# Kernel optimization log

Hardware: AMD Instinct MI355X
Metric: run time of the kernel (lower is better)

The kernel has to match this reference:

```python
import jax, jax.numpy as jnp
import numpy as np

N1 = 4096
N2 = 4096


def _encoder(x, w1, b1, w2, b2, w3, b3):
    # fc1 -> fc2 -> fc3 -> relu (relu only after fc3, matching the torch code)
    h = x @ w1.T + b1
    h = h @ w2.T + b2
    h = h @ w3.T + b3
    return jax.nn.relu(h)


def _self_attention(x, adj, alpha, W):
    # tmp_i = sum_j [adj_ij==1] * alpha_ij * W * x_j ; tmp_i /= deg_i ; tmp_i += x_i (only if deg_i != 0)
    a = (adj == 1).astype(x.dtype)          # [N, N]
    deg = a.sum(axis=1)                     # [N]
    agg = (a * alpha) @ x                   # [N, 64] masked weighted aggregation
    agg = agg * W[0, 0]
    safe_deg = jnp.maximum(deg, 1.0)
    out = agg / safe_deg[:, None] + x       # residual
    return jnp.where((deg != 0.0)[:, None], out, jnp.zeros_like(out))


def setup_inputs() -> dict:
    key = jax.random.key(0)
    ks = jax.random.split(key, 20)
    s = 0.02  # weight scale to keep activations sane through the 4096->256->128->64 MLP
    inp = {
        "x1": jax.random.normal(ks[0], (N1, N1), jnp.float32),
        "x2": jax.random.normal(ks[1], (N2, N2), jnp.float32),
        "adj1": jax.random.randint(ks[2], (N1, N1), 0, 2, jnp.int32),
        "adj2": jax.random.randint(ks[3], (N2, N2), 0, 2, jnp.int32),
        "e1_w1": jax.random.normal(ks[4], (256, N1), jnp.float32) * s,
        "e1_b1": jnp.zeros((256,), jnp.float32),
        "e1_w2": jax.random.normal(ks[5], (128, 256), jnp.float32) * s,
        "e1_b2": jnp.zeros((128,), jnp.float32),
        "e1_w3": jax.random.normal(ks[6], (64, 128), jnp.float32) * s,
        "e1_b3": jnp.zeros((64,), jnp.float32),
        "e2_w1": jax.random.normal(ks[7], (256, N2), jnp.float32) * s,
        "e2_b1": jnp.zeros((256,), jnp.float32),
        "e2_w2": jax.random.normal(ks[8], (128, 256), jnp.float32) * s,
        "e2_b2": jnp.zeros((128,), jnp.float32),
        "e2_w3": jax.random.normal(ks[9], (64, 128), jnp.float32) * s,
        "e2_b3": jnp.zeros((64,), jnp.float32),
        "W": jax.random.normal(ks[10], (1, 1), jnp.float32),
        "alpha1": jax.random.normal(ks[11], (N1, N1), jnp.float32),
        "clf_w": jax.random.normal(ks[12], (2, (N1 + N2) * 64), jnp.float32) * s,
        "clf_b": jnp.zeros((2,), jnp.float32),
    }
    return inp


def reference(x1, x2, adj1, adj2,
              e1_w1, e1_b1, e1_w2, e1_b2, e1_w3, e1_b3,
              e2_w1, e2_b1, e2_w2, e2_b2, e2_w3, e2_b3,
              W, alpha1, clf_w, clf_b):
    h1 = _encoder(x1, e1_w1, e1_b1, e1_w2, e1_b2, e1_w3, e1_b3)  # [N1, 64]
    h2 = _encoder(x2, e2_w1, e2_b1, e2_w2, e2_b2, e2_w3, e2_b3)  # [N2, 64]
    # NOTE: original torch code uses self.alpha1 for BOTH graphs (alpha2 is unused)
    new1 = _self_attention(h1, adj1, alpha1, W)
    new2 = _self_attention(h2, adj2, alpha1[:N2, :N2], W)
    feat = jnp.concatenate([new1, new2], axis=0).reshape(1, -1)  # [1, (N1+N2)*64]
    return feat @ clf_w.T + clf_b  # [1, 2]
```

## Files before the change

kernel.cpp:

```cpp
#include <hip/hip_runtime.h>
#include <hip/hip_bf16.h>
#include <stdint.h>

#define N 4096

typedef __attribute__((ext_vector_type(4))) float f32x4;
typedef __attribute__((ext_vector_type(8))) short s16x8;

__device__ inline unsigned short f2bf(float f) {
    unsigned int u = __float_as_uint(f);
    u += 0x7fffu + ((u >> 16) & 1u);
    return (unsigned short)(u >> 16);
}
__device__ inline float bf2f(unsigned short h) {
    return __uint_as_float(((unsigned int)h) << 16);
}

__global__ void k0a(const float* __restrict__ w2a, const float* __restrict__ w3a,
                    const float* __restrict__ b1a, const float* __restrict__ b2a, const float* __restrict__ b3a,
                    const float* __restrict__ w2b, const float* __restrict__ w3b,
                    const float* __restrict__ b1b, const float* __restrict__ b2b, const float* __restrict__ b3b,
                    float* __restrict__ T, float* __restrict__ beff) {
    const int g  = blockIdx.x >> 5;
    const int nb = blockIdx.x & 31;
    const float* w2 = g ? w2b : w2a;
    const float* w3 = g ? w3b : w3a;
    const int c  = threadIdx.x;
    const int n0 = nb * 2;
    float a0 = 0.f, a1 = 0.f;
#pragma unroll 8
    for (int r = 0; r < 128; ++r) {
        float w = w2[r * 256 + c];
        a0 += w3[n0 * 128 + r] * w;
        a1 += w3[n0 * 128 + 128 + r] * w;
    }
    float* Tg = T + g * 64 * 256;
    Tg[n0 * 256 + c]       = a0;
    Tg[(n0 + 1) * 256 + c] = a1;

    if (nb == 0) {
        __shared__ float u[128];
        const float* b1 = g ? b1b : b1a;
        const float* b2 = g ? b2b : b2a;
        const float* b3 = g ? b3b : b3a;
        if (threadIdx.x < 128) {
            int r = threadIdx.x;
            float s = 0.f;
            for (int cc = 0; cc < 256; ++cc) s += w2[r * 256 + cc] * b1[cc];
            u[r] = s + b2[r];
        }
        __syncthreads();
        if (threadIdx.x < 64) {
            int n = threadIdx.x;
            float s = 0.f;
            for (int r = 0; r < 128; ++r) s += w3[n * 128 + r] * u[r];
            beff[g * 64 + n] = s + b3[n];
        }
    }
}

__global__ void k0b(const float* __restrict__ w1a, const float* __restrict__ w1b,
                    const float* __restrict__ T,
                    unsigned short* __restrict__ Whi, unsigned short* __restrict__ Wlo) {
    const int b  = blockIdx.x;
    const int g  = b >> 7, n8 = (b >> 4) & 7, kc = b & 15;
    const float* w1 = g ? w1b : w1a;
    const float* Tg = T + (g * 64 + n8 * 8) * 256;
    const int kx = kc * 256 + threadIdx.x;
    float acc[8] = {0, 0, 0, 0, 0, 0, 0, 0};
#pragma unroll 8
    for (int r = 0; r < 256; ++r) {
        float w = w1[r * N + kx];
#pragma unroll
        for (int j = 0; j < 8; ++j) acc[j] += Tg[j * 256 + r] * w;
    }
#pragma unroll
    for (int j = 0; j < 8; ++j) {
        size_t idx = (size_t)(g * 64 + n8 * 8 + j) * N + kx;
        unsigned short hi = f2bf(acc[j]);
        Whi[idx] = hi;
        Wlo[idx] = f2bf(acc[j] - bf2f(hi));
    }
}

__global__ __launch_bounds__(256) void k1(const float* __restrict__ x1, const float* __restrict__ x2,
                                          const unsigned short* __restrict__ Whi,
                                          const unsigned short* __restrict__ Wlo,
                                          const float* __restrict__ beff,
                                          float* __restrict__ hf, unsigned short* __restrict__ hT) {
    const int b  = blockIdx.x;
    const int g  = b & 1;
    const int i0 = (b >> 1) * 16;
    const float* x = g ? x2 : x1;
    const size_t goff = (size_t)g * 64 * N;

    const int t = threadIdx.x;
    const int lane = t & 63, kg = t >> 6;
    const int q = lane >> 4, l15 = lane & 15;

    __shared__ float accs[4][4][64][4];

    f32x4 acc[4];
#pragma unroll
    for (int ng = 0; ng < 4; ++ng) acc[ng] = (f32x4){0.f, 0.f, 0.f, 0.f};

    const float* xrow = x + (size_t)(i0 + l15) * N;
    for (int kk = 0; kk < 16; ++kk) {
#pragma unroll
        for (int c = 0; c < 2; ++c) {
            const int ka = kg * 1024 + kk * 64 + c * 32 + q * 8;
            float4 a0 = *(const float4*)&xrow[ka];
            float4 a1 = *(const float4*)&xrow[ka + 4];
            s16x8 bh[4], bl[4];
#pragma unroll
            for (int ng = 0; ng < 4; ++ng) {
                const size_t bo = goff + (size_t)(ng * 16 + l15) * N + ka;
                bh[ng] = *(const s16x8*)&Whi[bo];
                bl[ng] = *(const s16x8*)&Wlo[bo];
            }
            float xv[8] = {a0.x, a0.y, a0.z, a0.w, a1.x, a1.y, a1.z, a1.w};
            s16x8 ah, al;
#pragma unroll
            for (int j = 0; j < 8; ++j) {
                unsigned short h = f2bf(xv[j]);
                ah[j] = (short)h;
                al[j] = (short)f2bf(xv[j] - bf2f(h));
            }
#pragma unroll
            for (int ng = 0; ng < 4; ++ng) {
                acc[ng] = __builtin_amdgcn_mfma_f32_16x16x32_bf16(al, bh[ng], acc[ng], 0, 0, 0);
                acc[ng] = __builtin_amdgcn_mfma_f32_16x16x32_bf16(ah, bl[ng], acc[ng], 0, 0, 0);
                acc[ng] = __builtin_amdgcn_mfma_f32_16x16x32_bf16(ah, bh[ng], acc[ng], 0, 0, 0);
            }
        }
    }
#pragma unroll
    for (int ng = 0; ng < 4; ++ng)
#pragma unroll
        for (int r = 0; r < 4; ++r) accs[kg][ng][lane][r] = acc[ng][r];
    __syncthreads();

    const int n = kg * 16 + l15;
    const float be = beff[g * 64 + n];
    unsigned short pk[4];
#pragma unroll
    for (int r = 0; r < 4; ++r) {
        float v = accs[0][kg][lane][r] + accs[1][kg][lane][r]
                + accs[2][kg][lane][r] + accs[3][kg][lane][r] + be;
        v = fmaxf(v, 0.f);
        hf[(size_t)(g * N + i0 + q * 4 + r) * 64 + n] = v;
        pk[r] = f2bf(v);
    }
    *(ushort4*)&hT[(size_t)(g * 64 + n) * N + i0 + q * 4] = make_ushort4(pk[0], pk[1], pk[2], pk[3]);
}

__global__ __launch_bounds__(256) void k2(const int* __restrict__ adj1, const int* __restrict__ adj2,
                                          const float* __restrict__ alpha, const float* __restrict__ Wp,
                                          const unsigned short* __restrict__ hT, const float* __restrict__ hf,
                                          float* __restrict__ outv) {
    const int i0 = blockIdx.x * 16;
    const int t = threadIdx.x;
    const int lane = t & 63, kg = t >> 6;
    const int q = lane >> 4, l15 = lane & 15;

    __shared__ float accs[4][4][64][8];
    __shared__ float degp[4][64][2];
    __shared__ float degf[2][16];

    f32x4 acc[4][2];
#pragma unroll
    for (int ng = 0; ng < 4; ++ng) {
        acc[ng][0] = (f32x4){0.f, 0.f, 0.f, 0.f};
        acc[ng][1] = (f32x4){0.f, 0.f, 0.f, 0.f};
    }
    int deg1 = 0, deg2 = 0;

    const size_t rowoff = (size_t)(i0 + l15) * N;
    for (int kk = 0; kk < 16; ++kk) {
#pragma unroll
        for (int c = 0; c < 2; ++c) {
            const int ka = kg * 1024 + kk * 64 + c * 32 + q * 8;
            const size_t ao = rowoff + ka;
            float4 a0 = *(const float4*)&alpha[ao];
            float4 a1 = *(const float4*)&alpha[ao + 4];
            int4 j10 = *(const int4*)&adj1[ao];
            int4 j11 = *(const int4*)&adj1[ao + 4];
            int4 j20 = *(const int4*)&adj2[ao];
            int4 j21 = *(const int4*)&adj2[ao + 4];
            s16x8 b1[4], b2[4];
#pragma unroll
            for (int ng = 0; ng < 4; ++ng) {
                const size_t bo = (size_t)(ng * 16 + l15) * N + ka;
                b1[ng] = *(const s16x8*)&hT[bo];
                b2[ng] = *(const s16x8*)&hT[(size_t)64 * N + bo];
            }
            float av[8] = {a0.x, a0.y, a0.z, a0.w, a1.x, a1.y, a1.z, a1.w};
            int m1[8] = {j10.x == 1, j10.y == 1, j10.z == 1, j10.w == 1,
                         j11.x == 1, j11.y == 1, j11.z == 1, j11.w == 1};
            int m2[8] = {j20.x == 1, j20.y == 1, j20.z == 1, j20.w == 1,
                         j21.x == 1, j21.y == 1, j21.z == 1, j21.w == 1};
            s16x8 af1, af2;
#pragma unroll
            for (int j = 0; j < 8; ++j) {
                short bv = (short)f2bf(av[j]);
                af1[j] = m1[j] ? bv : (short)0;
                af2[j] = m2[j] ? bv : (short)0;
                deg1 += m1[j];
                deg2 += m2[j];
            }
#pragma unroll
            for (int ng = 0; ng < 4; ++ng) {
                acc[ng][0] = __builtin_amdgcn_mfma_f32_16x16x32_bf16(af1, b1[ng], acc[ng][0], 0, 0, 0);
                acc[ng][1] = __builtin_amdgcn_mfma_f32_16x16x32_bf16(af2, b2[ng], acc[ng][1], 0, 0, 0);
            }
        }
    }
#pragma unroll
    for (int ng = 0; ng < 4; ++ng)
#pragma unroll
        for (int gg = 0; gg < 2; ++gg)
#pragma unroll
            for (int r = 0; r < 4; ++r) accs[kg][ng][lane][gg * 4 + r] = acc[ng][gg][r];
    degp[kg][lane][0] = (float)deg1;
    degp[kg][lane][1] = (float)deg2;
    __syncthreads();
    if (t < 32) {
        int gg = t >> 4, row = t & 15;
        float s = 0.f;
#pragma unroll
        for (int w = 0; w < 4; ++w)
#pragma unroll
            for (int qq = 0; qq < 4; ++qq) s += degp[w][qq * 16 + row][gg];
        degf[gg][row] = s;
    }
    __syncthreads();

    const float W00 = Wp[0];
    const int n = kg * 16 + l15;
#pragma unroll
    for (int r = 0; r < 4; ++r) {
        int iloc = q * 4 + r;
        int i = i0 + iloc;
        float s1 = accs[0][kg][lane][r] + accs[1][kg][lane][r]
                 + accs[2][kg][lane][r] + accs[3][kg][lane][r];
        float s2 = accs[0][kg][lane][4 + r] + accs[1][kg][lane][4 + r]
                 + accs[2][kg][lane][4 + r] + accs[3][kg][lane][4 + r];
        float dg1 = degf[0][iloc], dg2 = degf[1][iloc];
        float hv1 = hf[(size_t)i * 64 + n];
        outv[(size_t)i * 64 + n] = (dg1 != 0.f) ? (s1 * W00 / fmaxf(dg1, 1.f) + hv1) : 0.f;
        float hv2 = hf[(size_t)(N + i) * 64 + n];
        outv[(size_t)(N + i) * 64 + n] = (dg2 != 0.f) ? (s2 * W00 / fmaxf(dg2, 1.f) + hv2) : 0.f;
    }
}

__global__ __launch_bounds__(256) void k3a(const float* __restrict__ feat, const float* __restrict__ clfw,
                                           float* __restrict__ part) {
    const int t = threadIdx.x;
    const size_t idx = (size_t)blockIdx.x * 2048 + (size_t)t * 8;
    float4 a0 = *(const float4*)&feat[idx];
    float4 a1 = *(const float4*)&feat[idx + 4];
    float4 c0 = *(const float4*)&clfw[idx];
    float4 c1 = *(const float4*)&clfw[idx + 4];
    float4 d0 = *(const float4*)&clfw[524288 + idx];
    float4 d1 = *(const float4*)&clfw[524288 + idx + 4];
    float s0 = a0.x * c0.x + a0.y * c0.y + a0.z * c0.z + a0.w * c0.w
             + a1.x * c1.x + a1.y * c1.y + a1.z * c1.z + a1.w * c1.w;
    float s1 = a0.x * d0.x + a0.y * d0.y + a0.z * d0.z + a0.w * d0.w
             + a1.x * d1.x + a1.y * d1.y + a1.z * d1.z + a1.w * d1.w;
    __shared__ float r0[256], r1[256];
    r0[t] = s0; r1[t] = s1;
    __syncthreads();
    for (int s = 128; s > 0; s >>= 1) {
        if (t < s) { r0[t] += r0[t + s]; r1[t] += r1[t + s]; }
        __syncthreads();
    }
    if (t == 0) { part[blockIdx.x * 2] = r0[0]; part[blockIdx.x * 2 + 1] = r1[0]; }
}

__global__ void k3b(const float* __restrict__ part, const float* __restrict__ clfb,
                    float* __restrict__ outp) {
    const int t = threadIdx.x;
    __shared__ float r0[256], r1[256];
    r0[t] = part[t * 2]; r1[t] = part[t * 2 + 1];
    __syncthreads();
    for (int s = 128; s > 0; s >>= 1) {
        if (t < s) { r0[t] += r0[t + s]; r1[t] += r1[t + s]; }
        __syncthreads();
    }
    if (t == 0) { outp[0] = r0[0] + clfb[0]; outp[1] = r1[0] + clfb[1]; }
}

extern "C" void kernel_launch(void* const* d_in, const int* in_sizes, int n_in,
                              void* d_out, int out_size, void* d_ws, size_t ws_size,
                              hipStream_t stream) {
    const float* x1   = (const float*)d_in[0];
    const float* x2   = (const float*)d_in[1];
    const int*   adj1 = (const int*)d_in[2];
    const int*   adj2 = (const int*)d_in[3];
    const float* e1w1 = (const float*)d_in[4];
    const float* e1b1 = (const float*)d_in[5];
    const float* e1w2 = (const float*)d_in[6];
    const float* e1b2 = (const float*)d_in[7];
    const float* e1w3 = (const float*)d_in[8];
    const float* e1b3 = (const float*)d_in[9];
    const float* e2w1 = (const float*)d_in[10];
    const float* e2b1 = (const float*)d_in[11];
    const float* e2w2 = (const float*)d_in[12];
    const float* e2b2 = (const float*)d_in[13];
    const float* e2w3 = (const float*)d_in[14];
    const float* e2b3 = (const float*)d_in[15];
    const float* Wp   = (const float*)d_in[16];
    const float* alph = (const float*)d_in[17];
    const float* clfw = (const float*)d_in[18];
    const float* clfb = (const float*)d_in[19];

    char* wsb = (char*)d_ws;
    unsigned short* Whi = (unsigned short*)(wsb);
    unsigned short* Wlo = (unsigned short*)(wsb + (1u << 20));
    float* newv = (float*)(wsb);
    unsigned short* hT  = (unsigned short*)(wsb + (2u << 20));
    float* hf   = (float*)(wsb + (3u << 20));
    float* T    = (float*)(wsb + (5u << 20));
    float* beff = (float*)(wsb + (5u << 20) + (1u << 17));
    float* part = (float*)(wsb + (5u << 20) + (1u << 17) + 4096);

    hipLaunchKernelGGL(k0a, dim3(64), dim3(256), 0, stream,
                       e1w2, e1w3, e1b1, e1b2, e1b3, e2w2, e2w3, e2b1, e2b2, e2b3, T, beff);
    hipLaunchKernelGGL(k0b, dim3(256), dim3(256), 0, stream, e1w1, e2w1, T, Whi, Wlo);
    hipLaunchKernelGGL(k1, dim3(512), dim3(256), 0, stream, x1, x2, Whi, Wlo, beff, hf, hT);
    hipLaunchKernelGGL(k2, dim3(256), dim3(256), 0, stream, adj1, adj2, alph, Wp, hT, hf, newv);
    hipLaunchKernelGGL(k3a, dim3(256), dim3(256), 0, stream, newv, clfw, part);
    hipLaunchKernelGGL(k3b, dim3(1), dim3(256), 0, stream, part, clfb, (float*)d_out);
}
```

Measured before the change: 455.3 us.

## Store weights and hidden features in MFMA fragment layout, double warps per block

The folded first-layer weights (hi/lo bf16) and the transposed bf16 hidden features are now written in a pre-swizzled MFMA fragment order. Each lane then loads its operand as one contiguous 16-byte chunk instead of strided rows. k1 and k2 move from 4 to 8 waves per block, each wave covering a smaller K slice, with an 8-way LDS reduction. k2 also swaps the MFMA operand roles and reduces the two graphs one after the other to save LDS. The aim is better memory coalescing and more parallelism, in exchange for extra synchronisation and reduction work.

```diff
diff --git a/kernel.cpp b/kernel.cpp
--- a/kernel.cpp
+++ b/kernel.cpp
@@ -59,64 +59,91 @@
     }
 }
 
-__global__ void k0b(const float* __restrict__ w1a, const float* __restrict__ w1b,
-                    const float* __restrict__ T,
-                    unsigned short* __restrict__ Whi, unsigned short* __restrict__ Wlo) {
+__global__ __launch_bounds__(256) void k0b(const float* __restrict__ w1a, const float* __restrict__ w1b,
+                                           const float* __restrict__ T,
+                                           unsigned short* __restrict__ Wfrag) {
     const int b  = blockIdx.x;
-    const int g  = b >> 7, n8 = (b >> 4) & 7, kc = b & 15;
+    const int g  = b >> 6, kc = b & 63;
     const float* w1 = g ? w1b : w1a;
-    const float* Tg = T + (g * 64 + n8 * 8) * 256;
-    const int kx = kc * 256 + threadIdx.x;
-    float acc[8] = {0, 0, 0, 0, 0, 0, 0, 0};
-#pragma unroll 8
+    const int t = threadIdx.x;
+    const int ng = t >> 6, lane = t & 63;
+    const int q = lane >> 4, l15 = lane & 15;
+    const float* Trow = T + (size_t)(g * 64 + ng * 16 + l15) * 256;
+    const int kx0 = kc * 64 + q * 8;
+
+    float acc[2][8];
+#pragma unroll
+    for (int c = 0; c < 2; ++c)
+#pragma unroll
+        for (int j = 0; j < 8; ++j) acc[c][j] = 0.f;
+
+#pragma unroll 4
     for (int r = 0; r < 256; ++r) {
-        float w = w1[r * N + kx];
-#pragma unroll
-        for (int j = 0; j < 8; ++j) acc[j] += Tg[j * 256 + r] * w;
-    }
-#pragma unroll
-    for (int j = 0; j < 8; ++j) {
-        size_t idx = (size_t)(g * 64 + n8 * 8 + j) * N + kx;
-        unsigned short hi = f2bf(acc[j]);
-        Whi[idx] = hi;
-        Wlo[idx] = f2bf(acc[j] - bf2f(hi));
-    }
-}
-
-__global__ __launch_bounds__(256) void k1(const float* __restrict__ x1, const float* __restrict__ x2,
-                                          const unsigned short* __restrict__ Whi,
-                                          const unsigned short* __restrict__ Wlo,
-                                          const float* __restrict__ beff,
-                                          float* __restrict__ hf, unsigned short* __restrict__ hT) {
+        float tv = Trow[r];
+        const float* wr = w1 + (size_t)r * N + kx0;
+        float4 wa = *(const float4*)&wr[0];
+        float4 wb = *(const float4*)&wr[4];
+        float4 wc = *(const float4*)&wr[32];
+        float4 wd = *(const float4*)&wr[36];
+        acc[0][0] += tv * wa.x; acc[0][1] += tv * wa.y; acc[0][2] += tv * wa.z; acc[0][3] += tv * wa.w;
+        acc[0][4] += tv * wb.x; acc[0][5] += tv * wb.y; acc[0][6] += tv * wb.z; acc[0][7] += tv * wb.w;
+        acc[1][0] += tv * wc.x; acc[1][1] += tv * wc.y; acc[1][2] += tv * wc.z; acc[1][3] += tv * wc.w;
+        acc[1][4] += tv * wd.x; acc[1][5] += tv * wd.y; acc[1][6] += tv * wd.z; acc[1][7] += tv * wd.w;
+    }
+
+#pragma unroll
+    for (int c = 0; c < 2; ++c) {
+        unsigned short hi[8], lo[8];
+#pragma unroll
+        for (int j = 0; j < 8; ++j) {
+            hi[j] = f2bf(acc[c][j]);
+            lo[j] = f2bf(acc[c][j] - bf2f(hi[j]));
+        }
+        const size_t unit = ((((size_t)g * 64 + kc) * 4 + ng) * 2 + c) * 2;
+        uint4 hp, lp;
+        hp.x = (unsigned)hi[0] | ((unsigned)hi[1] << 16); hp.y = (unsigned)hi[2] | ((unsigned)hi[3] << 16);
+        hp.z = (unsigned)hi[4] | ((unsigned)hi[5] << 16); hp.w = (unsigned)hi[6] | ((unsigned)hi[7] << 16);
+        lp.x = (unsigned)lo[0] | ((unsigned)lo[1] << 16); lp.y = (unsigned)lo[2] | ((unsigned)lo[3] << 16);
+        lp.z = (unsigned)lo[4] | ((unsigned)lo[5] << 16); lp.w = (unsigned)lo[6] | ((unsigned)lo[7] << 16);
+        *(uint4*)&Wfrag[unit * 512 + lane * 8]       = hp;
+        *(uint4*)&Wfrag[(unit + 1) * 512 + lane * 8] = lp;
+    }
+}
+
+__global__ __launch_bounds__(512, 4) void k1(const float* __restrict__ x1, const float* __restrict__ x2,
+                                             const unsigned short* __restrict__ Wfrag,
+                                             const float* __restrict__ beff,
+                                             float* __restrict__ hf, unsigned short* __restrict__ hfrag) {
     const int b  = blockIdx.x;
     const int g  = b & 1;
     const int i0 = (b >> 1) * 16;
     const float* x = g ? x2 : x1;
-    const size_t goff = (size_t)g * 64 * N;
 
     const int t = threadIdx.x;
     const int lane = t & 63, kg = t >> 6;
     const int q = lane >> 4, l15 = lane & 15;
 
-    __shared__ float accs[4][4][64][4];
+    __shared__ float accs[8][4][64][4];
+    __shared__ unsigned short htile[64][16];
 
     f32x4 acc[4];
 #pragma unroll
     for (int ng = 0; ng < 4; ++ng) acc[ng] = (f32x4){0.f, 0.f, 0.f, 0.f};
 
     const float* xrow = x + (size_t)(i0 + l15) * N;
-    for (int kk = 0; kk < 16; ++kk) {
+    for (int kk = 0; kk < 8; ++kk) {
+        const int kc = kg * 8 + kk;
 #pragma unroll
         for (int c = 0; c < 2; ++c) {
-            const int ka = kg * 1024 + kk * 64 + c * 32 + q * 8;
+            const int ka = kc * 64 + c * 32 + q * 8;
             float4 a0 = *(const float4*)&xrow[ka];
             float4 a1 = *(const float4*)&xrow[ka + 4];
             s16x8 bh[4], bl[4];
 #pragma unroll
             for (int ng = 0; ng < 4; ++ng) {
-                const size_t bo = goff + (size_t)(ng * 16 + l15) * N + ka;
-                bh[ng] = *(const s16x8*)&Whi[bo];
-                bl[ng] = *(const s16x8*)&Wlo[bo];
+                const size_t unit = ((((size_t)g * 64 + kc) * 4 + ng) * 2 + c) * 2;
+                bh[ng] = *(const s16x8*)&Wfrag[unit * 512 + lane * 8];
+                bl[ng] = *(const s16x8*)&Wfrag[(unit + 1) * 512 + lane * 8];
             }
             float xv[8] = {a0.x, a0.y, a0.z, a0.w, a1.x, a1.y, a1.z, a1.w};
             s16x8 ah, al;
@@ -140,46 +167,61 @@
         for (int r = 0; r < 4; ++r) accs[kg][ng][lane][r] = acc[ng][r];
     __syncthreads();
 
-    const int n = kg * 16 + l15;
-    const float be = beff[g * 64 + n];
-    unsigned short pk[4];
-#pragma unroll
-    for (int r = 0; r < 4; ++r) {
-        float v = accs[0][kg][lane][r] + accs[1][kg][lane][r]
-                + accs[2][kg][lane][r] + accs[3][kg][lane][r] + be;
-        v = fmaxf(v, 0.f);
-        hf[(size_t)(g * N + i0 + q * 4 + r) * 64 + n] = v;
-        pk[r] = f2bf(v);
-    }
-    *(ushort4*)&hT[(size_t)(g * 64 + n) * N + i0 + q * 4] = make_ushort4(pk[0], pk[1], pk[2], pk[3]);
-}
-
-__global__ __launch_bounds__(256) void k2(const int* __restrict__ adj1, const int* __restrict__ adj2,
-                                          const float* __restrict__ alpha, const float* __restrict__ Wp,
-                                          const unsigned short* __restrict__ hT, const float* __restrict__ hf,
-                                          float* __restrict__ outv) {
+    {
+        const int ng = kg & 3, rh = kg >> 2;
+        const int n = ng * 16 + l15;
+        const float be = beff[g * 64 + n];
+#pragma unroll
+        for (int rr = 0; rr < 2; ++rr) {
+            const int r = rh * 2 + rr;
+            float s = 0.f;
+#pragma unroll
+            for (int k8 = 0; k8 < 8; ++k8) s += accs[k8][ng][lane][r];
+            float v = fmaxf(s + be, 0.f);
+            const int il = q * 4 + r;
+            hf[(size_t)(g * N + i0 + il) * 64 + n] = v;
+            htile[n][il] = f2bf(v);
+        }
+    }
+    __syncthreads();
+
+    if (t < 128) {
+        const int ng2 = t >> 5, jh = (t >> 4) & 1, l = t & 15;
+        uint4 v = *(const uint4*)&htile[ng2 * 16 + l][jh * 8];
+        const int jc = i0 >> 6, c = (i0 >> 5) & 1, q0 = (i0 >> 3) & 3;
+        const size_t unit = (((size_t)g * 4 + ng2) * 64 + jc) * 2 + c;
+        *(uint4*)&hfrag[unit * 512 + (size_t)(q0 + jh) * 128 + l * 8] = v;
+    }
+}
+
+__global__ __launch_bounds__(512, 2) void k2(const int* __restrict__ adj1, const int* __restrict__ adj2,
+                                             const float* __restrict__ alpha, const float* __restrict__ Wp,
+                                             const unsigned short* __restrict__ hfrag,
+                                             const float* __restrict__ hf,
+                                             float* __restrict__ outv) {
     const int i0 = blockIdx.x * 16;
     const int t = threadIdx.x;
     const int lane = t & 63, kg = t >> 6;
     const int q = lane >> 4, l15 = lane & 15;
 
-    __shared__ float accs[4][4][64][8];
-    __shared__ float degp[4][64][2];
+    __shared__ float accs[8][4][64][4];
+    __shared__ float degp[8][64][2];
     __shared__ float degf[2][16];
 
-    f32x4 acc[4][2];
+    f32x4 acc1[4], acc2[4];
 #pragma unroll
     for (int ng = 0; ng < 4; ++ng) {
-        acc[ng][0] = (f32x4){0.f, 0.f, 0.f, 0.f};
-        acc[ng][1] = (f32x4){0.f, 0.f, 0.f, 0.f};
+        acc1[ng] = (f32x4){0.f, 0.f, 0.f, 0.f};
+        acc2[ng] = (f32x4){0.f, 0.f, 0.f, 0.f};
     }
     int deg1 = 0, deg2 = 0;
 
     const size_t rowoff = (size_t)(i0 + l15) * N;
-    for (int kk = 0; kk < 16; ++kk) {
+    for (int kk = 0; kk < 8; ++kk) {
+        const int jc = kg * 8 + kk;
 #pragma unroll
         for (int c = 0; c < 2; ++c) {
-            const int ka = kg * 1024 + kk * 64 + c * 32 + q * 8;
+            const int ka = jc * 64 + c * 32 + q * 8;
             const size_t ao = rowoff + ka;
             float4 a0 = *(const float4*)&alpha[ao];
             float4 a1 = *(const float4*)&alpha[ao + 4];
@@ -187,48 +229,48 @@
             int4 j11 = *(const int4*)&adj1[ao + 4];
             int4 j20 = *(const int4*)&adj2[ao];
             int4 j21 = *(const int4*)&adj2[ao + 4];
-            s16x8 b1[4], b2[4];
+            s16x8 ha1[4], ha2[4];
 #pragma unroll
             for (int ng = 0; ng < 4; ++ng) {
-                const size_t bo = (size_t)(ng * 16 + l15) * N + ka;
-                b1[ng] = *(const s16x8*)&hT[bo];
-                b2[ng] = *(const s16x8*)&hT[(size_t)64 * N + bo];
+                const size_t u1 = (((size_t)0 * 4 + ng) * 64 + jc) * 2 + c;
+                const size_t u2 = (((size_t)1 * 4 + ng) * 64 + jc) * 2 + c;
+                ha1[ng] = *(const s16x8*)&hfrag[u1 * 512 + lane * 8];
+                ha2[ng] = *(const s16x8*)&hfrag[u2 * 512 + lane * 8];
             }
             float av[8] = {a0.x, a0.y, a0.z, a0.w, a1.x, a1.y, a1.z, a1.w};
             int m1[8] = {j10.x == 1, j10.y == 1, j10.z == 1, j10.w == 1,
                          j11.x == 1, j11.y == 1, j11.z == 1, j11.w == 1};
             int m2[8] = {j20.x == 1, j20.y == 1, j20.z == 1, j20.w == 1,
                          j21.x == 1, j21.y == 1, j21.z == 1, j21.w == 1};
-            s16x8 af1, af2;
+            s16x8 bf1, bf2;
 #pragma unroll
             for (int j = 0; j < 8; ++j) {
                 short bv = (short)f2bf(av[j]);
-                af1[j] = m1[j] ? bv : (short)0;
-                af2[j] = m2[j] ? bv : (short)0;
+                bf1[j] = m1[j] ? bv : (short)0;
+                bf2[j] = m2[j] ? bv : (short)0;
                 deg1 += m1[j];
                 deg2 += m2[j];
             }
 #pragma unroll
             for (int ng = 0; ng < 4; ++ng) {
-                acc[ng][0] = __builtin_amdgcn_mfma_f32_16x16x32_bf16(af1, b1[ng], acc[ng][0], 0, 0, 0);
-                acc[ng][1] = __builtin_amdgcn_mfma_f32_16x16x32_bf16(af2, b2[ng], acc[ng][1], 0, 0, 0);
-            }
-        }
-    }
-#pragma unroll
-    for (int ng = 0; ng < 4; ++ng)
-#pragma unroll
-        for (int gg = 0; gg < 2; ++gg)
-#pragma unroll
-            for (int r = 0; r < 4; ++r) accs[kg][ng][lane][gg * 4 + r] = acc[ng][gg][r];
+                acc1[ng] = __builtin_amdgcn_mfma_f32_16x16x32_bf16(ha1[ng], bf1, acc1[ng], 0, 0, 0);
+                acc2[ng] = __builtin_amdgcn_mfma_f32_16x16x32_bf16(ha2[ng], bf2, acc2[ng], 0, 0, 0);
+            }
+        }
+    }
+
     degp[kg][lane][0] = (float)deg1;
     degp[kg][lane][1] = (float)deg2;
+#pragma unroll
+    for (int ng = 0; ng < 4; ++ng)
+#pragma unroll
+        for (int r = 0; r < 4; ++r) accs[kg][ng][lane][r] = acc1[ng][r];
     __syncthreads();
     if (t < 32) {
         int gg = t >> 4, row = t & 15;
         float s = 0.f;
 #pragma unroll
-        for (int w = 0; w < 4; ++w)
+        for (int w = 0; w < 8; ++w)
 #pragma unroll
             for (int qq = 0; qq < 4; ++qq) s += degp[w][qq * 16 + row][gg];
         degf[gg][row] = s;
@@ -236,20 +278,41 @@
     __syncthreads();
 
     const float W00 = Wp[0];
-    const int n = kg * 16 + l15;
-#pragma unroll
-    for (int r = 0; r < 4; ++r) {
-        int iloc = q * 4 + r;
-        int i = i0 + iloc;
-        float s1 = accs[0][kg][lane][r] + accs[1][kg][lane][r]
-                 + accs[2][kg][lane][r] + accs[3][kg][lane][r];
-        float s2 = accs[0][kg][lane][4 + r] + accs[1][kg][lane][4 + r]
-                 + accs[2][kg][lane][4 + r] + accs[3][kg][lane][4 + r];
-        float dg1 = degf[0][iloc], dg2 = degf[1][iloc];
-        float hv1 = hf[(size_t)i * 64 + n];
-        outv[(size_t)i * 64 + n] = (dg1 != 0.f) ? (s1 * W00 / fmaxf(dg1, 1.f) + hv1) : 0.f;
-        float hv2 = hf[(size_t)(N + i) * 64 + n];
-        outv[(size_t)(N + i) * 64 + n] = (dg2 != 0.f) ? (s2 * W00 / fmaxf(dg2, 1.f) + hv2) : 0.f;
+    {
+        const int ng = kg & 3, rh = kg >> 2;
+        const int i = i0 + l15;
+        const float dg = degf[0][l15];
+#pragma unroll
+        for (int rr = 0; rr < 2; ++rr) {
+            const int r = rh * 2 + rr;
+            float s = 0.f;
+#pragma unroll
+            for (int k8 = 0; k8 < 8; ++k8) s += accs[k8][ng][lane][r];
+            const int n = ng * 16 + q * 4 + r;
+            float hv = hf[(size_t)i * 64 + n];
+            outv[(size_t)i * 64 + n] = (dg != 0.f) ? (s * W00 / fmaxf(dg, 1.f) + hv) : 0.f;
+        }
+    }
+    __syncthreads();
+#pragma unroll
+    for (int ng = 0; ng < 4; ++ng)
+#pragma unroll
+        for (int r = 0; r < 4; ++r) accs[kg][ng][lane][r] = acc2[ng][r];
+    __syncthreads();
+    {
+        const int ng = kg & 3, rh = kg >> 2;
+        const int i = i0 + l15;
+        const float dg = degf[1][l15];
+#pragma unroll
+        for (int rr = 0; rr < 2; ++rr) {
+            const int r = rh * 2 + rr;
+            float s = 0.f;
+#pragma unroll
+            for (int k8 = 0; k8 < 8; ++k8) s += accs[k8][ng][lane][r];
+            const int n = ng * 16 + q * 4 + r;
+            float hv = hf[(size_t)(N + i) * 64 + n];
+            outv[(size_t)(N + i) * 64 + n] = (dg != 0.f) ? (s * W00 / fmaxf(dg, 1.f) + hv) : 0.f;
+        }
     }
 }
 
@@ -315,10 +378,9 @@
     const float* clfb = (const float*)d_in[19];
 
     char* wsb = (char*)d_ws;
-    unsigned short* Whi = (unsigned short*)(wsb);
-    unsigned short* Wlo = (unsigned short*)(wsb + (1u << 20));
+    unsigned short* Wfrag = (unsigned short*)(wsb);
     float* newv = (float*)(wsb);
-    unsigned short* hT  = (unsigned short*)(wsb + (2u << 20));
+    unsigned short* hfrag = (unsigned short*)(wsb + (2u << 20));
     float* hf   = (float*)(wsb + (3u << 20));
     float* T    = (float*)(wsb + (5u << 20));
     float* beff = (float*)(wsb + (5u << 20) + (1u << 17));
@@ -326,9 +388,9 @@
 
     hipLaunchKernelGGL(k0a, dim3(64), dim3(256), 0, stream,
                        e1w2, e1w3, e1b1, e1b2, e1b3, e2w2, e2w3, e2b1, e2b2, e2b3, T, beff);
-    hipLaunchKernelGGL(k0b, dim3(256), dim3(256), 0, stream, e1w1, e2w1, T, Whi, Wlo);
-    hipLaunchKernelGGL(k1, dim3(512), dim3(256), 0, stream, x1, x2, Whi, Wlo, beff, hf, hT);
-    hipLaunchKernelGGL(k2, dim3(256), dim3(256), 0, stream, adj1, adj2, alph, Wp, hT, hf, newv);
+    hipLaunchKernelGGL(k0b, dim3(128), dim3(256), 0, stream, e1w1, e2w1, T, Wfrag);
+    hipLaunchKernelGGL(k1, dim3(512), dim3(512), 0, stream, x1, x2, Wfrag, beff, hf, hfrag);
+    hipLaunchKernelGGL(k2, dim3(256), dim3(512), 0, stream, adj1, adj2, alph, Wp, hfrag, hf, newv);
     hipLaunchKernelGGL(k3a, dim3(256), dim3(256), 0, stream, newv, clfw, part);
     hipLaunchKernelGGL(k3b, dim3(1), dim3(256), 0, stream, part, clfb, (float*)d_out);
 }
```

Result: no change. 460.0 us (+1.0%).
